# Kernel optimization log

Hardware: AMD Instinct MI355X
Metric: run time of the kernel (lower is better)

## Reference

```python
import jax, jax.numpy as jnp
import numpy as np

B, S, HID = 2, 4096, 2048
NH, NKV, HD = 16, 4, 128  # num_heads, num_kv_heads, head_dim
GROUPS = NH // NKV
ROPE_THETA = 10000.0


def _rope_cos_sin(position_ids):
    # position_ids: [B, S] int
    inv_freq = 1.0 / (ROPE_THETA ** (jnp.arange(0, HD, 2, dtype=jnp.float32) / HD))  # [HD/2]
    freqs = position_ids.astype(jnp.float32)[..., None] * inv_freq  # [B, S, HD/2]
    emb = jnp.concatenate([freqs, freqs], axis=-1)  # [B, S, HD]
    return jnp.cos(emb), jnp.sin(emb)


def _rotate_half(x):
    x1, x2 = jnp.split(x, 2, axis=-1)
    return jnp.concatenate([-x2, x1], axis=-1)


def _apply_rope(q, k, cos, sin):
    # q: [B, NH, S, HD], k: [B, NKV, S, HD]; cos/sin: [B, S, HD]
    cos = cos[:, None, :, :]
    sin = sin[:, None, :, :]
    q = q * cos + _rotate_half(q) * sin
    k = k * cos + _rotate_half(k) * sin
    return q, k


def kappa(x):
    return jax.nn.elu(x) + 1.0


def setup_inputs() -> dict:
    key = jax.random.key(0)
    ks = jax.random.split(key, 8)
    sc = 0.02
    hidden_states = jax.random.normal(ks[0], (B, S, HID), dtype=jnp.float32)
    position_ids = jnp.broadcast_to(jnp.arange(S, dtype=jnp.int64)[None, :], (B, S))
    Wq = jax.random.normal(ks[1], (HID, NH * HD), dtype=jnp.float32) * sc
    Wk = jax.random.normal(ks[2], (HID, NKV * HD), dtype=jnp.float32) * sc
    Wv = jax.random.normal(ks[3], (HID, NKV * HD), dtype=jnp.float32) * sc
    Wo = jax.random.normal(ks[4], (HID, HID), dtype=jnp.float32) * sc
    Wphi = jax.random.normal(ks[5], (HID, HID), dtype=jnp.float32) * sc
    bphi = jax.random.normal(ks[6], (HID,), dtype=jnp.float32) * sc
    return {"hidden_states": hidden_states, "position_ids": position_ids,
            "Wq": Wq, "Wk": Wk, "Wv": Wv, "Wo": Wo, "Wphi": Wphi, "bphi": bphi}


def reference(hidden_states, position_ids, Wq, Wk, Wv, Wo, Wphi, bphi):
    b, s, _ = hidden_states.shape
    # projections -> [B, heads, S, HD]
    q = (hidden_states @ Wq).reshape(b, s, NH, HD).transpose(0, 2, 1, 3)
    k = (hidden_states @ Wk).reshape(b, s, NKV, HD).transpose(0, 2, 1, 3)
    v = (hidden_states @ Wv).reshape(b, s, NKV, HD).transpose(0, 2, 1, 3)
    cos, sin = _rope_cos_sin(position_ids)
    q, k = _apply_rope(q, k, cos, sin)
    # GQA expand kv heads
    k = jnp.repeat(k, GROUPS, axis=1)  # [B, NH, S, HD]
    v = jnp.repeat(v, GROUPS, axis=1)
    Qk = kappa(q)
    Kk = kappa(k)
    Qg = Qk.mean(axis=2)  # [B, NH, HD]
    logits = jnp.einsum('bnd,bnsd->bns', Qg, Kk)
    alpha = jax.nn.softmax(logits, axis=-1) * float(s)  # [B, NH, S]
    outer_sum = jnp.einsum('bns,bnsd,bnsf->bndf', alpha, Kk, v)  # [B, NH, HD, HD]
    X_phi = (hidden_states @ Wphi + bphi).reshape(b, s, NH, HD).transpose(0, 2, 1, 3)
    result_attn = jnp.einsum('bnsd,bndf->bnsf', Qk, outer_sum)
    context = (X_phi * result_attn).transpose(0, 2, 1, 3).reshape(b, s, HID)
    return context @ Wo
```

## Files before the change

kernel.cpp:

```cpp
#include <hip/hip_runtime.h>
#include <hip/hip_bf16.h>
#include <math.h>

#define B_    2
#define S_    4096
#define HID_  2048
#define NH_   16
#define NKV_  4
#define HD_   128
#define GROUPS_ (NH_/NKV_)
#define ROPE_THETA_ 10000.0f
#define OSPLIT 8
#define QCH   32

typedef __attribute__((ext_vector_type(8))) short short8;
typedef __attribute__((ext_vector_type(4))) float f32x4;

__device__ inline unsigned short f2bf(float f) {
    __hip_bfloat16 h = __float2bfloat16(f);
    return *(unsigned short*)&h;
}

__device__ inline float bf2f(short u) {
    union { unsigned int i; float f; } v;
    v.i = ((unsigned int)(unsigned short)u) << 16;
    return v.f;
}

__device__ inline void gload16(const void* g, void* l) {
    __builtin_amdgcn_global_load_lds((const __attribute__((address_space(1))) void*)g,
                                     (__attribute__((address_space(3))) void*)l, 16, 0, 0);
}

#define BARM() asm volatile("s_barrier" ::: "memory")

__global__ void rope_table_kernel(float* __restrict__ cosT, float* __restrict__ sinT) {
    int s = blockIdx.x;
    int i = threadIdx.x;
    float expo = -2.0f * (float)i / (float)HD_;
    float invf = powf(ROPE_THETA_, expo);
    float f = (float)s * invf;
    cosT[s * 64 + i] = cosf(f);
    sinT[s * 64 + i] = sinf(f);
}

__global__ void cast_bf16_kernel(const float* __restrict__ in,
                                 __hip_bfloat16* __restrict__ out, int n8) {
    int i = blockIdx.x * 256 + threadIdx.x;
    if (i >= n8) return;
    const float4 v0 = *reinterpret_cast<const float4*>(&in[i * 8]);
    const float4 v1 = *reinterpret_cast<const float4*>(&in[i * 8 + 4]);
    union { short8 v; unsigned short u[8]; } o;
    o.u[0] = f2bf(v0.x); o.u[1] = f2bf(v0.y); o.u[2] = f2bf(v0.z); o.u[3] = f2bf(v0.w);
    o.u[4] = f2bf(v1.x); o.u[5] = f2bf(v1.y); o.u[6] = f2bf(v1.z); o.u[7] = f2bf(v1.w);
    *reinterpret_cast<short8*>(&out[i * 8]) = o.v;
}

__global__ __launch_bounds__(256) void transpose_cast_all_kernel(
        const float* __restrict__ W0, const float* __restrict__ W1,
        const float* __restrict__ W2, const float* __restrict__ W3,
        const float* __restrict__ W4, __hip_bfloat16* __restrict__ dstBase) {
    __shared__ float T[64][65];
    int id = blockIdx.x;
    const float* W; int N; size_t dof;
    if (id < 1024)      { W = W0; N = 2048; dof = 0; }
    else if (id < 1280) { W = W1; N = 512;  dof = (size_t)2048 * HID_;                  id -= 1024; }
    else if (id < 1536) { W = W2; N = 512;  dof = (size_t)(2048 + 512) * HID_;          id -= 1280; }
    else if (id < 2560) { W = W3; N = 2048; dof = (size_t)(2048 + 1024) * HID_;         id -= 1536; }
    else                { W = W4; N = 2048; dof = (size_t)(4096 + 1024) * HID_;         id -= 2560; }
    __hip_bfloat16* Wt = dstBase + dof;
    int nb = N >> 6;
    int n0 = (id % nb) * 64, k0 = (id / nb) * 64;
    int tid = threadIdx.x;
    int r = tid >> 4, c4 = (tid & 15) * 4;
#pragma unroll
    for (int p = 0; p < 4; ++p) {
        float4 v = *reinterpret_cast<const float4*>(&W[(size_t)(k0 + r + p * 16) * N + n0 + c4]);
        T[r + p * 16][c4 + 0] = v.x;
        T[r + p * 16][c4 + 1] = v.y;
        T[r + p * 16][c4 + 2] = v.z;
        T[r + p * 16][c4 + 3] = v.w;
    }
    __syncthreads();
#pragma unroll
    for (int p = 0; p < 4; ++p) {
        int n = r + p * 16;
        short4 o;
        o.x = (short)f2bf(T[c4 + 0][n]);
        o.y = (short)f2bf(T[c4 + 1][n]);
        o.z = (short)f2bf(T[c4 + 2][n]);
        o.w = (short)f2bf(T[c4 + 3][n]);
        *reinterpret_cast<short4*>(&Wt[(size_t)(n0 + n) * HID_ + k0 + c4]) = o;
    }
}

__device__ __forceinline__ void stage_region128(const __hip_bfloat16* __restrict__ src,
        int ldK, int row0, int kbase, __hip_bfloat16* dst, int tid) {
#pragma unroll
    for (int g = 0; g < 2; ++g) {
        int P = g * 256 + tid;
        int row = P >> 2, cp = P & 3;
        int cl = cp ^ ((row >> 1) & 3);
        gload16(src + (size_t)(row0 + row) * ldK + kbase + cl * 8, dst + P * 8);
    }
}

#define BM 128
#define BN 128
#define T128EL 8192
__global__ __launch_bounds__(256) void gemm_mfma_kernel(
        const __hip_bfloat16* __restrict__ A, const __hip_bfloat16* __restrict__ Bt,
        float* __restrict__ C, __hip_bfloat16* __restrict__ Cb,
        const float* __restrict__ bias, int M, int N, int K) {
    __shared__ __hip_bfloat16 lds[4 * T128EL];
    int tid  = threadIdx.x;
    int wid  = tid >> 6, lane = tid & 63;
    int wr   = wid >> 1, wc = wid & 1;
    int lr = lane & 15, lc = lane >> 4;
    int c16 = lc ^ ((lr >> 1) & 3);
    int bm = blockIdx.y * BM, bn = blockIdx.x * BN;

    f32x4 acc[4][4];
#pragma unroll
    for (int m = 0; m < 4; ++m)
#pragma unroll
        for (int n = 0; n < 4; ++n)
#pragma unroll
            for (int i = 0; i < 4; ++i) acc[m][n][i] = 0.0f;

    const int NKT = K >> 5;

    stage_region128(A,  K, bm, 0,  lds,                 tid);
    stage_region128(Bt, K, bn, 0,  lds + 4096,          tid);
    stage_region128(A,  K, bm, 32, lds + T128EL,        tid);
    stage_region128(Bt, K, bn, 32, lds + T128EL + 4096, tid);
    asm volatile("s_waitcnt vmcnt(4)" ::: "memory");
    BARM();

    for (int kt = 0; kt < NKT; ++kt) {
        __hip_bfloat16* buf = lds + (size_t)(kt & 3) * T128EL;
        __hip_bfloat16* stg = lds + (size_t)((kt + 2) & 3) * T128EL;
        const bool pf = (kt + 2 < NKT);
        if (pf) {
            stage_region128(A,  K, bm, (kt + 2) << 5, stg,        tid);
            stage_region128(Bt, K, bn, (kt + 2) << 5, stg + 4096, tid);
        }
        short8 af[4], bf[4];
#pragma unroll
        for (int m = 0; m < 4; ++m)
            af[m] = *reinterpret_cast<const short8*>(
                &buf[(size_t)(wr * 64 + m * 16 + lr) * 32 + c16 * 8]);
#pragma unroll
        for (int n = 0; n < 4; ++n)
            bf[n] = *reinterpret_cast<const short8*>(
                &buf[4096 + (size_t)(wc * 64 + n * 16 + lr) * 32 + c16 * 8]);
        __builtin_amdgcn_s_setprio(1);
#pragma unroll
        for (int m = 0; m < 4; ++m)
#pragma unroll
            for (int n = 0; n < 4; ++n)
                acc[m][n] = __builtin_amdgcn_mfma_f32_16x16x32_bf16(
                    af[m], bf[n], acc[m][n], 0, 0, 0);
        __builtin_amdgcn_s_setprio(0);
        if (pf) { asm volatile("s_waitcnt vmcnt(4)" ::: "memory"); }
        else    { asm volatile("s_waitcnt vmcnt(0)" ::: "memory"); }
        BARM();
    }

    int lq = lane >> 4;
#pragma unroll
    for (int m = 0; m < 4; ++m) {
#pragma unroll
        for (int n = 0; n < 4; ++n) {
            int row = bm + wr * 64 + m * 16 + lq * 4;
            int col = bn + wc * 64 + n * 16 + lr;
            float bv = (bias != nullptr) ? bias[col] : 0.0f;
            if (Cb != nullptr) {
#pragma unroll
                for (int r = 0; r < 4; ++r)
                    Cb[(size_t)(row + r) * N + col] = __float2bfloat16(acc[m][n][r] + bv);
            } else {
#pragma unroll
                for (int r = 0; r < 4; ++r)
                    C[(size_t)(row + r) * N + col] = acc[m][n][r] + bv;
            }
        }
    }
}

#define HBUF 32768

__device__ __forceinline__ void stageA64(const __hip_bfloat16* __restrict__ A,
        int ldK, int bm, int k0, __hip_bfloat16* dst, int g, int tid) {
    int P = g * 512 + tid;
    int row = P >> 3, sp = P & 7;
    gload16(A + (size_t)(bm + row) * ldK + k0 + ((sp ^ (row & 7)) << 3),
            dst + (size_t)P * 8);
}
__device__ __forceinline__ void stageB64(const __hip_bfloat16* __restrict__ Bt,
        int ldK, int bn, int k0, __hip_bfloat16* dst, int g, int tid) {
    int P = g * 512 + tid;
    int row = P >> 3, sp = P & 7;
    gload16(Bt + (size_t)(bn + row) * ldK + k0 + ((sp ^ (row & 7)) << 3),
            dst + 16384 + (size_t)P * 8);
}

__device__ __forceinline__ short8 ldsA64(const __hip_bfloat16* buf, int row, int slot_log) {
    int sp = slot_log ^ (row & 7);
    return *reinterpret_cast<const short8*>(&buf[(size_t)row * 64 + sp * 8]);
}
__device__ __forceinline__ short8 ldsB64(const __hip_bfloat16* buf, int row, int slot_log) {
    int sp = slot_log ^ (row & 7);
    return *reinterpret_cast<const short8*>(&buf[16384 + (size_t)row * 64 + sp * 8]);
}

__global__ __launch_bounds__(512, 2) void gemm_mfma256_kernel(
        const __hip_bfloat16* __restrict__ A, const __hip_bfloat16* __restrict__ Bt,
        float* __restrict__ C, __hip_bfloat16* __restrict__ Cb,
        const float* __restrict__ bias, int M, int N, int K) {
    __shared__ __hip_bfloat16 lds[2 * HBUF];
    int tid = threadIdx.x, lane = tid & 63, wid = tid >> 6;
    int wr = wid >> 2, wc = wid & 3;
    int lr = lane & 15, lc = lane >> 4;

    int nwg = gridDim.x;
    int orig = blockIdx.x;
    int q = nwg >> 3, r = nwg & 7;
    int xcd = orig & 7, lid = orig >> 3;
    int wg = (xcd < r ? xcd * (q + 1) : r * (q + 1) + (xcd - r) * q) + lid;
    int tiles_n = N >> 8;
    int bm = (wg / tiles_n) << 8, bn = (wg % tiles_n) << 8;

    f32x4 acc[8][4];
#pragma unroll
    for (int m = 0; m < 8; ++m)
#pragma unroll
        for (int n = 0; n < 4; ++n)
#pragma unroll
            for (int i = 0; i < 4; ++i) acc[m][n][i] = 0.0f;

    const int NKT = K >> 6;
    __hip_bfloat16* buf0 = lds;
    __hip_bfloat16* buf1 = lds + HBUF;

#pragma unroll
    for (int g = 0; g < 4; ++g) stageA64(A, K, bm, 0, buf0, g, tid);
#pragma unroll
    for (int g = 0; g < 4; ++g) stageB64(Bt, K, bn, 0, buf0, g, tid);
    stageA64(A, K, bm, 64, buf1, 0, tid);
    stageA64(A, K, bm, 64, buf1, 1, tid);
    asm volatile("s_waitcnt vmcnt(2)" ::: "memory");
    BARM();

    for (int kt = 0; kt < NKT; ++kt) {
        __hip_bfloat16* buf = (kt & 1) ? buf1 : buf0;
        __hip_bfloat16* nxt = (kt & 1) ? buf0 : buf1;
        const bool p1 = (kt + 1 < NKT), p2 = (kt + 2 < NKT);
        const int kn1 = (kt + 1) << 6;

        short8 al[4], ah[4], bl[2], bh[2];

#pragma unroll
        for (int kk = 0; kk < 2; ++kk) {
            int sl = kk * 4 + lc;
#pragma unroll
            for (int m = 0; m < 4; ++m)
                al[m] = ldsA64(buf, wr * 128 + m * 16 + lr, sl);
#pragma unroll
            for (int n = 0; n < 2; ++n)
                bl[n] = ldsB64(buf, wc * 64 + n * 16 + lr, sl);
            if (kk == 0 && p1) {
                stageA64(A, K, bm, kn1, nxt, 2, tid);
                stageA64(A, K, bm, kn1, nxt, 3, tid);
                stageB64(Bt, K, bn, kn1, nxt, 0, tid);
            }
            BARM();
            __builtin_amdgcn_s_setprio(1);
#pragma unroll
            for (int m = 0; m < 4; ++m)
#pragma unroll
                for (int n = 0; n < 2; ++n)
                    acc[m][n] = __builtin_amdgcn_mfma_f32_16x16x32_bf16(
                        al[m], bl[n], acc[m][n], 0, 0, 0);
            __builtin_amdgcn_s_setprio(0);
            BARM();
#pragma unroll
            for (int m = 0; m < 4; ++m)
                ah[m] = ldsA64(buf, wr * 128 + 64 + m * 16 + lr, sl);
            if (kk == 0 && p1) {
                stageB64(Bt, K, bn, kn1, nxt, 1, tid);
                stageB64(Bt, K, bn, kn1, nxt, 2, tid);
                stageB64(Bt, K, bn, kn1, nxt, 3, tid);
            }
            BARM();
            __builtin_amdgcn_s_setprio(1);
#pragma unroll
            for (int m = 0; m < 4; ++m)
#pragma unroll
                for (int n = 0; n < 2; ++n)
                    acc[m + 4][n] = __builtin_amdgcn_mfma_f32_16x16x32_bf16(
                        ah[m], bl[n], acc[m + 4][n], 0, 0, 0);
            __builtin_amdgcn_s_setprio(0);
            BARM();
#pragma unroll
            for (int n = 0; n < 2; ++n)
                bh[n] = ldsB64(buf, wc * 64 + (n + 2) * 16 + lr, sl);
            BARM();
            __builtin_amdgcn_s_setprio(1);
#pragma unroll
            for (int m = 0; m < 4; ++m)
#pragma unroll
                for (int n = 0; n < 2; ++n)
                    acc[m][n + 2] = __builtin_amdgcn_mfma_f32_16x16x32_bf16(
                        al[m], bh[n], acc[m][n + 2], 0, 0, 0);
            __builtin_amdgcn_s_setprio(0);
            BARM();
            if (kk == 1 && p2) {
                stageA64(A, K, bm, (kt + 2) << 6, buf, 0, tid);
                stageA64(A, K, bm, (kt + 2) << 6, buf, 1, tid);
            }
            __builtin_amdgcn_s_setprio(1);
#pragma unroll
            for (int m = 0; m < 4; ++m)
#pragma unroll
                for (int n = 0; n < 2; ++n)
                    acc[m + 4][n + 2] = __builtin_amdgcn_mfma_f32_16x16x32_bf16(
                        ah[m], bh[n], acc[m + 4][n + 2], 0, 0, 0);
            __builtin_amdgcn_s_setprio(0);
            if (kk == 1) {
                if (p2)      { asm volatile("s_waitcnt vmcnt(2)" ::: "memory"); }
                else if (p1) { asm volatile("s_waitcnt vmcnt(0)" ::: "memory"); }
                BARM();
            } else {
                BARM();
            }
        }
    }

    int lq = lane >> 4;
#pragma unroll
    for (int m = 0; m < 8; ++m) {
#pragma unroll
        for (int n = 0; n < 4; ++n) {
            int row = bm + wr * 128 + m * 16 + lq * 4;
            int col = bn + wc * 64 + n * 16 + lr;
            float bv = (bias != nullptr) ? bias[col] : 0.0f;
            if (Cb != nullptr) {
#pragma unroll
                for (int rr = 0; rr < 4; ++rr)
                    Cb[(size_t)(row + rr) * N + col] = __float2bfloat16(acc[m][n][rr] + bv);
            } else {
#pragma unroll
                for (int rr = 0; rr < 4; ++rr)
                    C[(size_t)(row + rr) * N + col] = acc[m][n][rr] + bv;
            }
        }
    }
}

__global__ void rope_kappa_b_kernel(__hip_bfloat16* __restrict__ Xb,
                                    const float* __restrict__ cosT,
                                    const float* __restrict__ sinT,
                                    int nheads, int rs, int total) {
    int idx = blockIdx.x * 256 + threadIdx.x;
    if (idx >= total) return;
    int dq = idx & 15;
    int t  = idx >> 4;
    int n  = t % nheads;
    int bs = t / nheads;
    int s  = bs % S_;
    size_t base = (size_t)bs * rs + n * HD_ + dq * 4;
    short4 v1 = *reinterpret_cast<short4*>(&Xb[base]);
    short4 v2 = *reinterpret_cast<short4*>(&Xb[base + 64]);
    float4 c4 = *reinterpret_cast<const float4*>(&cosT[s * 64 + dq * 4]);
    float4 s4 = *reinterpret_cast<const float4*>(&sinT[s * 64 + dq * 4]);
    float x1[4] = {bf2f(v1.x), bf2f(v1.y), bf2f(v1.z), bf2f(v1.w)};
    float x2[4] = {bf2f(v2.x), bf2f(v2.y), bf2f(v2.z), bf2f(v2.w)};
    float cc[4] = {c4.x, c4.y, c4.z, c4.w};
    float ss[4] = {s4.x, s4.y, s4.z, s4.w};
    short r1s[4], r2s[4];
#pragma unroll
    for (int j = 0; j < 4; ++j) {
        float r1 = x1[j] * cc[j] - x2[j] * ss[j];
        float r2 = x2[j] * cc[j] + x1[j] * ss[j];
        r1 = (r1 > 0.0f) ? (r1 + 1.0f) : expf(r1);
        r2 = (r2 > 0.0f) ? (r2 + 1.0f) : expf(r2);
        r1s[j] = (short)f2bf(r1);
        r2s[j] = (short)f2bf(r2);
    }
    short4 o1, o2;
    o1.x = r1s[0]; o1.y = r1s[1]; o1.z = r1s[2]; o1.w = r1s[3];
    o2.x = r2s[0]; o2.y = r2s[1]; o2.z = r2s[2]; o2.w = r2s[3];
    *reinterpret_cast<short4*>(&Xb[base])      = o1;
    *reinterpret_cast<short4*>(&Xb[base + 64]) = o2;
}

__global__ __launch_bounds__(256) void qg_partial_kernel(
        const __hip_bfloat16* __restrict__ Qb, float* __restrict__ QPART) {
    int blk = blockIdx.x;
    int c   = blk % QCH;
    int bn  = blk / QCH;
    int b = bn / NH_, n = bn % NH_;
    int t = threadIdx.x;
    int d8 = (t & 15) * 8;
    int sg = t >> 4;
    float acc[8] = {};
    int s0 = c * (S_ / QCH);
    for (int s = s0 + sg; s < s0 + S_ / QCH; s += 16) {
        short8 v = *reinterpret_cast<const short8*>(
            &Qb[((size_t)b * S_ + s) * (NH_ * HD_) + n * HD_ + d8]);
#pragma unroll
        for (int j = 0; j < 8; ++j) acc[j] += bf2f(v[j]);
    }
    __shared__ float red[16][128];
#pragma unroll
    for (int j = 0; j < 8; ++j) red[sg][d8 + j] = acc[j];
    __syncthreads();
    if (t < 128) {
        float s = 0.0f;
#pragma unroll
        for (int g = 0; g < 16; ++g) s += red[g][t];
        QPART[(size_t)(c * (B_ * NH_) + bn) * HD_ + t] = s;
    }
}

__global__ __launch_bounds__(256) void qg_reduce_kernel(
        const float* __restrict__ QPART, float* __restrict__ QG) {
    int idx = blockIdx.x * 256 + threadIdx.x;
    float acc = 0.0f;
#pragma unroll
    for (int c = 0; c < QCH; ++c)
        acc += QPART[(size_t)c * (B_ * NH_ * HD_) + idx];
    QG[idx] = acc * (1.0f / (float)S_);
}

__global__ __launch_bounds__(256) void logits_kernel(
        const __hip_bfloat16* __restrict__ KVb, const float* __restrict__ QG,
        float* __restrict__ LG) {
    int bk = blockIdx.x;
    int b = bk / NKV_, kn = bk % NKV_;
    int s0 = blockIdx.y * 256;
    int w = threadIdx.x >> 6, lane = threadIdx.x & 63;
    float2 qv[GROUPS_];
#pragma unroll
    for (int g = 0; g < GROUPS_; ++g)
        qv[g] = *reinterpret_cast<const float2*>(
            &QG[(size_t)(b * NH_ + kn * GROUPS_ + g) * HD_ + lane * 2]);
    for (int i = 0; i < 64; ++i) {
        int s = s0 + w * 64 + i;
        short2 kv = *reinterpret_cast<const short2*>(
            &KVb[((size_t)b * S_ + s) * 1024 + kn * HD_ + lane * 2]);
        float kx = bf2f(kv.x), ky = bf2f(kv.y);
        float p[GROUPS_];
#pragma unroll
        for (int g = 0; g < GROUPS_; ++g) p[g] = kx * qv[g].x + ky * qv[g].y;
#pragma unroll
        for (int off = 32; off > 0; off >>= 1)
#pragma unroll
            for (int g = 0; g < GROUPS_; ++g) p[g] += __shfl_xor(p[g], off);
        if (lane == 0) {
#pragma unroll
            for (int g = 0; g < GROUPS_; ++g)
                LG[(size_t)(b * NH_ + kn * GROUPS_ + g) * S_ + s] = p[g];
        }
    }
}

__global__ __launch_bounds__(1024) void softmax_alpha_kernel(float* __restrict__ LG) {
    int bn = blockIdx.x;
    float* row = &LG[(size_t)bn * S_];
    __shared__ float lg[S_];
    __shared__ float red[1024];
    int tid = threadIdx.x;
    float lmax = -1e30f;
    for (int s = tid; s < S_; s += 1024) {
        float v = row[s];
        lg[s] = v;
        lmax = fmaxf(lmax, v);
    }
    red[tid] = lmax;
    __syncthreads();
    for (int off = 512; off > 0; off >>= 1) {
        if (tid < off) red[tid] = fmaxf(red[tid], red[tid + off]);
        __syncthreads();
    }
    float mx = red[0];
    __syncthreads();
    float lsum = 0.0f;
    for (int s = tid; s < S_; s += 1024) {
        float e = expf(lg[s] - mx);
        lg[s] = e;
        lsum += e;
    }
    red[tid] = lsum;
    __syncthreads();
    for (int off = 512; off > 0; off >>= 1) {
        if (tid < off) red[tid] += red[tid + off];
        __syncthreads();
    }
    float inv = (float)S_ / red[0];
    for (int s = tid; s < S_; s += 1024)
        row[s] = lg[s] * inv;
}

__global__ __launch_bounds__(256) void kvt_kernel(
        const __hip_bfloat16* __restrict__ KVb, const float* __restrict__ ALPHA,
        __hip_bfloat16* __restrict__ AKT, __hip_bfloat16* __restrict__ VT) {
    int bk = blockIdx.x;
    int b = bk / NKV_, kn = bk % NKV_;
    int s0 = blockIdx.y * 64;
    int isV = blockIdx.z;
    __shared__ float T[64][HD_ + 4];
    __shared__ float alf[GROUPS_][64];
    int tid = threadIdx.x;

    int r = tid >> 2;
    int c0 = (tid & 3) * 32;
    const __hip_bfloat16* src =
        KVb + ((size_t)(b * S_) + s0 + r) * 1024 + isV * 512 + kn * HD_ + c0;
#pragma unroll
    for (int i = 0; i < 4; ++i) {
        short8 v = *reinterpret_cast<const short8*>(src + i * 8);
#pragma unroll
        for (int j = 0; j < 8; ++j) T[r][c0 + i * 8 + j] = bf2f(v[j]);
    }
    if (!isV) {
        int g = tid >> 6, ss = tid & 63;
        alf[g][ss] = ALPHA[(size_t)(b * NH_ + kn * GROUPS_ + g) * S_ + s0 + ss];
    }
    __syncthreads();

    int d  = tid >> 1;
    int sh = (tid & 1) * 32;
    if (isV) {
        __hip_bfloat16* dst = VT + ((size_t)bk * HD_ + d) * S_ + s0 + sh;
#pragma unroll
        for (int i = 0; i < 8; ++i) {
            short4 o;
            o.x = (short)f2bf(T[sh + i * 4 + 0][d]);
            o.y = (short)f2bf(T[sh + i * 4 + 1][d]);
            o.z = (short)f2bf(T[sh + i * 4 + 2][d]);
            o.w = (short)f2bf(T[sh + i * 4 + 3][d]);
            *reinterpret_cast<short4*>(dst + i * 4) = o;
        }
    } else {
#pragma unroll
        for (int g = 0; g < GROUPS_; ++g) {
            int n = kn * GROUPS_ + g;
            __hip_bfloat16* dst = AKT + ((size_t)(b * NH_ + n) * HD_ + d) * S_ + s0 + sh;
#pragma unroll
            for (int i = 0; i < 8; ++i) {
                short4 o;
                o.x = (short)f2bf(T[sh + i * 4 + 0][d] * alf[g][sh + i * 4 + 0]);
                o.y = (short)f2bf(T[sh + i * 4 + 1][d] * alf[g][sh + i * 4 + 1]);
                o.z = (short)f2bf(T[sh + i * 4 + 2][d] * alf[g][sh + i * 4 + 2]);
                o.w = (short)f2bf(T[sh + i * 4 + 3][d] * alf[g][sh + i * 4 + 3]);
                *reinterpret_cast<short4*>(dst + i * 4) = o;
            }
        }
    }
}

__global__ __launch_bounds__(256) void outer_mfma_kernel(
        const __hip_bfloat16* __restrict__ AKT, const __hip_bfloat16* __restrict__ VT,
        float* __restrict__ OPT) {
    int bn = blockIdx.x;
    int sp = blockIdx.y;
    int b = bn / NH_, n = bn % NH_;
    int kn = n / GROUPS_;
    const __hip_bfloat16* Abase = AKT + (size_t)bn * HD_ * S_ + sp * (S_ / OSPLIT);
    const __hip_bfloat16* Bbase = VT + (size_t)(b * NKV_ + kn) * HD_ * S_ + sp * (S_ / OSPLIT);
    __shared__ __hip_bfloat16 As[128 * 32];
    __shared__ __hip_bfloat16 Bs[128 * 32];
    int tid = threadIdx.x, lane = tid & 63, wid = tid >> 6;
    int wr = wid >> 1, wc = wid & 1;
    int lr = lane & 15, kq = (lane >> 4) * 8;

    f32x4 acc[4][4];
#pragma unroll
    for (int m = 0; m < 4; ++m)
#pragma unroll
        for (int nn = 0; nn < 4; ++nn)
#pragma unroll
            for (int i = 0; i < 4; ++i) acc[m][nn][i] = 0.0f;

    for (int ks = 0; ks < (S_ / OSPLIT) / 32; ++ks) {
        int k0 = ks * 32;
#pragma unroll
        for (int g = 0; g < 2; ++g) {
            int P = g * 256 + tid;
            int row = P >> 2, gr = P & 3;
            gload16(Abase + (size_t)row * S_ + k0 + gr * 8, As + P * 8);
            gload16(Bbase + (size_t)row * S_ + k0 + gr * 8, Bs + P * 8);
        }
        __syncthreads();
        short8 af[4], bf[4];
#pragma unroll
        for (int m = 0; m < 4; ++m)
            af[m] = *reinterpret_cast<short8*>(&As[(wr * 64 + m * 16 + lr) * 32 + kq]);
#pragma unroll
        for (int nn = 0; nn < 4; ++nn)
            bf[nn] = *reinterpret_cast<short8*>(&Bs[(wc * 64 + nn * 16 + lr) * 32 + kq]);
#pragma unroll
        for (int m = 0; m < 4; ++m)
#pragma unroll
            for (int nn = 0; nn < 4; ++nn)
                acc[m][nn] = __builtin_amdgcn_mfma_f32_16x16x32_bf16(
                    af[m], bf[nn], acc[m][nn], 0, 0, 0);
        __syncthreads();
    }

    float* base = OPT + ((size_t)bn * OSPLIT + sp) * (HD_ * HD_);
    int lq = lane >> 4;
#pragma unroll
    for (int m = 0; m < 4; ++m) {
#pragma unroll
        for (int nn = 0; nn < 4; ++nn) {
            int drow = wr * 64 + m * 16 + lq * 4;
            int fcol = wc * 64 + nn * 16 + lr;
            float4 o;
            o.x = acc[m][nn][0]; o.y = acc[m][nn][1];
            o.z = acc[m][nn][2]; o.w = acc[m][nn][3];
            *reinterpret_cast<float4*>(&base[(size_t)fcol * HD_ + drow]) = o;
        }
    }
}

__global__ __launch_bounds__(256) void outer_reduce_tc_kernel(
        const float* __restrict__ OPT, __hip_bfloat16* __restrict__ OUTt) {
    int idx = blockIdx.x * 256 + threadIdx.x;
    int bn = idx >> 11;
    int rem = idx & 2047;
    int f = rem >> 4, g = rem & 15;
    const float* src = OPT + (size_t)bn * OSPLIT * 16384 + f * 128 + g * 8;
    float s[8] = {};
#pragma unroll
    for (int sp = 0; sp < OSPLIT; ++sp) {
        float4 v0 = *reinterpret_cast<const float4*>(src + (size_t)sp * 16384);
        float4 v1 = *reinterpret_cast<const float4*>(src + (size_t)sp * 16384 + 4);
        s[0] += v0.x; s[1] += v0.y; s[2] += v0.z; s[3] += v0.w;
        s[4] += v1.x; s[5] += v1.y; s[6] += v1.z; s[7] += v1.w;
    }
    int gp = g ^ (f & 7);
    union { short8 v; unsigned short u[8]; } o;
#pragma unroll
    for (int j = 0; j < 8; ++j) o.u[j] = f2bf(s[j]);
    *reinterpret_cast<short8*>(&OUTt[(size_t)bn * 16384 + f * 128 + gp * 8]) = o.v;
}

__global__ __launch_bounds__(256) void attn_context_mfma_kernel(
        const __hip_bfloat16* __restrict__ Qb, const __hip_bfloat16* __restrict__ OUTt,
        const __hip_bfloat16* __restrict__ XPHIb, __hip_bfloat16* __restrict__ CTX) {
    int bn = blockIdx.x;
    int b = bn / NH_, n = bn % NH_;
    int s0 = blockIdx.y * 256;
    __shared__ __hip_bfloat16 Ms[128 * 128];
    int tid = threadIdx.x, lane = tid & 63, wid = tid >> 6;
    int lr = lane & 15, lc = lane >> 4;

#pragma unroll
    for (int g = 0; g < 8; ++g) {
        int P = g * 256 + tid;
        gload16(OUTt + (size_t)bn * 16384 + (size_t)P * 8, Ms + (size_t)P * 8);
    }

    f32x4 acc[4][8];
#pragma unroll
    for (int m = 0; m < 4; ++m)
#pragma unroll
        for (int nn = 0; nn < 8; ++nn)
#pragma unroll
            for (int i = 0; i < 4; ++i) acc[m][nn][i] = 0.0f;

    __syncthreads();

    const __hip_bfloat16* qbase =
        Qb + ((size_t)(b * S_) + s0 + wid * 64) * (NH_ * HD_) + n * HD_;
#pragma unroll
    for (int ks = 0; ks < 4; ++ks) {
        int k8 = ks * 32 + lc * 8;
        short8 a[4];
#pragma unroll
        for (int m = 0; m < 4; ++m)
            a[m] = *reinterpret_cast<const short8*>(
                qbase + (size_t)(m * 16 + lr) * (NH_ * HD_) + k8);
        int gfull = ks * 4 + lc;
        short8 bb[8];
#pragma unroll
        for (int nn = 0; nn < 8; ++nn) {
            int f = nn * 16 + lr;
            int gp = gfull ^ (f & 7);
            bb[nn] = *reinterpret_cast<const short8*>(&Ms[f * 128 + gp * 8]);
        }
#pragma unroll
        for (int m = 0; m < 4; ++m)
#pragma unroll
            for (int nn = 0; nn < 8; ++nn)
                acc[m][nn] = __builtin_amdgcn_mfma_f32_16x16x32_bf16(
                    a[m], bb[nn], acc[m][nn], 0, 0, 0);
    }

#pragma unroll
    for (int m = 0; m < 4; ++m) {
#pragma unroll
        for (int nn = 0; nn < 8; ++nn) {
            int row = s0 + wid * 64 + m * 16 + lc * 4;
            int f = nn * 16 + lr;
            size_t gi = ((size_t)(b * S_) + row) * (NH_ * HD_) + n * HD_ + f;
#pragma unroll
            for (int r = 0; r < 4; ++r) {
                float xp = __bfloat162float(XPHIb[gi + (size_t)r * (NH_ * HD_)]);
                CTX[gi + (size_t)r * (NH_ * HD_)] = __float2bfloat16(acc[m][nn][r] * xp);
            }
        }
    }
}

extern "C" void kernel_launch(void* const* d_in, const int* in_sizes, int n_in,
                              void* d_out, int out_size, void* d_ws, size_t ws_size,
                              hipStream_t stream) {
    (void)in_sizes; (void)n_in; (void)out_size; (void)ws_size;
    const float* X    = (const float*)d_in[0];
    const float* Wq   = (const float*)d_in[2];
    const float* Wk   = (const float*)d_in[3];
    const float* Wv   = (const float*)d_in[4];
    const float* Wo   = (const float*)d_in[5];
    const float* Wphi = (const float*)d_in[6];
    const float* bphi = (const float*)d_in[7];
    float* out = (float*)d_out;

    float* ws = (float*)d_ws;
    const size_t nQ = (size_t)B_ * S_ * NH_ * HD_;
    const size_t nK = (size_t)B_ * S_ * NKV_ * HD_;
    float* Q     = ws;
    float* KV    = Q + nQ;
    float* XPHI  = KV + 2 * nK;
    float* QG    = XPHI + nQ;
    float* ALPHA = QG + (size_t)B_ * NH_ * HD_;
    float* QPART = ALPHA + (size_t)B_ * NH_ * S_;
    float* COST  = QPART + (size_t)QCH * B_ * NH_ * HD_;
    float* SINT  = COST + (size_t)S_ * 64;
    __hip_bfloat16* Xb    = (__hip_bfloat16*)(SINT + (size_t)S_ * 64);
    __hip_bfloat16* Wqt   = Xb + nQ;
    __hip_bfloat16* Wkt   = Wqt + (size_t)HID_ * (NH_ * HD_);
    __hip_bfloat16* Wvt   = Wkt + (size_t)HID_ * (NKV_ * HD_);
    __hip_bfloat16* Wphit = Wvt + (size_t)HID_ * (NKV_ * HD_);
    __hip_bfloat16* Wot   = Wphit + (size_t)HID_ * (NH_ * HD_);
    __hip_bfloat16* OUTt  = Wot + (size_t)HID_ * HID_;
    __hip_bfloat16* VT    = OUTt + (size_t)B_ * NH_ * HD_ * HD_;
    float* OPT = (float*)(VT + nK);
    __hip_bfloat16* Qb    = (__hip_bfloat16*)Q;
    __hip_bfloat16* KVb   = (__hip_bfloat16*)KV;
    __hip_bfloat16* CTXb  = (__hip_bfloat16*)KV;
    __hip_bfloat16* AKT   = Xb;
    __hip_bfloat16* XPHIb = (__hip_bfloat16*)XPHI;

    const int M = B_ * S_;

    rope_table_kernel<<<S_, 64, 0, stream>>>(COST, SINT);
    cast_bf16_kernel<<<(int)(nQ / 8 / 256), 256, 0, stream>>>(X, Xb, (int)(nQ / 8));
    transpose_cast_all_kernel<<<3584, 256, 0, stream>>>(Wq, Wk, Wv, Wphi, Wo, Wqt);

    gemm_mfma256_kernel<<<(M / 256) * ((NH_ * HD_) / 256), 512, 0, stream>>>(
        Xb, Wqt, nullptr, Qb, nullptr, M, NH_ * HD_, HID_);
    gemm_mfma_kernel<<<dim3(1024 / BN, M / BM), 256, 0, stream>>>(
        Xb, Wkt, nullptr, KVb, nullptr, M, 1024, HID_);
    gemm_mfma256_kernel<<<(M / 256) * ((NH_ * HD_) / 256), 512, 0, stream>>>(
        Xb, Wphit, nullptr, XPHIb, bphi, M, NH_ * HD_, HID_);

    {
        int totalQ = B_ * S_ * NH_ * 16;
        rope_kappa_b_kernel<<<totalQ / 256, 256, 0, stream>>>(
            Qb, COST, SINT, NH_, NH_ * HD_, totalQ);
        int totalK = B_ * S_ * NKV_ * 16;
        rope_kappa_b_kernel<<<totalK / 256, 256, 0, stream>>>(
            KVb, COST, SINT, NKV_, 1024, totalK);
    }

    qg_partial_kernel<<<B_ * NH_ * QCH, 256, 0, stream>>>(Qb, QPART);
    qg_reduce_kernel<<<(B_ * NH_ * HD_) / 256, 256, 0, stream>>>(QPART, QG);
    logits_kernel<<<dim3(B_ * NKV_, S_ / 256), 256, 0, stream>>>(KVb, QG, ALPHA);
    softmax_alpha_kernel<<<B_ * NH_, 1024, 0, stream>>>(ALPHA);

    kvt_kernel<<<dim3(B_ * NKV_, S_ / 64, 2), 256, 0, stream>>>(KVb, ALPHA, AKT, VT);
    outer_mfma_kernel<<<dim3(B_ * NH_, OSPLIT), 256, 0, stream>>>(AKT, VT, OPT);
    outer_reduce_tc_kernel<<<(B_ * NH_ * HD_ * 16) / 256, 256, 0, stream>>>(OPT, OUTt);

    attn_context_mfma_kernel<<<dim3(B_ * NH_, S_ / 256), 256, 0, stream>>>(
        Qb, OUTt, XPHIb, CTXb);

    gemm_mfma256_kernel<<<(M / 256) * (HID_ / 256), 512, 0, stream>>>(
        CTXb, Wot, out, nullptr, nullptr, M, HID_, HID_);
}
```

Before: 419.2 us.

## Merge Q and Xphi projections into one GEMM and fuse RoPE-kappa with Q mean

Q and Wphi weights are now transposed into one contiguous [4096 x HID] bf16 matrix, so a single 256x256-tile GEMM with N=4096 computes both projections. The epilogue sends each column tile to the Q or Xphi buffer and adds the bias only on the Xphi half. Separately, the Q RoPE+kappa pass is fused with the per-chunk Q column partial sums, which removes one full read of Q. The intent is to cut a kernel launch and a tail wave and to avoid re-reading the large Q tensor. The cost is a per-tile branch in the epilogue and a less coalesced access pattern in the fused RoPE kernel.

```diff
diff --git a/kernel.cpp b/kernel.cpp
--- a/kernel.cpp
+++ b/kernel.cpp
@@ -57,17 +57,17 @@
 }
 
 __global__ __launch_bounds__(256) void transpose_cast_all_kernel(
-        const float* __restrict__ W0, const float* __restrict__ W1,
-        const float* __restrict__ W2, const float* __restrict__ W3,
-        const float* __restrict__ W4, __hip_bfloat16* __restrict__ dstBase) {
+        const float* __restrict__ Wq, const float* __restrict__ Wphi,
+        const float* __restrict__ Wk, const float* __restrict__ Wv,
+        const float* __restrict__ Wo, __hip_bfloat16* __restrict__ dstBase) {
     __shared__ float T[64][65];
     int id = blockIdx.x;
     const float* W; int N; size_t dof;
-    if (id < 1024)      { W = W0; N = 2048; dof = 0; }
-    else if (id < 1280) { W = W1; N = 512;  dof = (size_t)2048 * HID_;                  id -= 1024; }
-    else if (id < 1536) { W = W2; N = 512;  dof = (size_t)(2048 + 512) * HID_;          id -= 1280; }
-    else if (id < 2560) { W = W3; N = 2048; dof = (size_t)(2048 + 1024) * HID_;         id -= 1536; }
-    else                { W = W4; N = 2048; dof = (size_t)(4096 + 1024) * HID_;         id -= 2560; }
+    if (id < 1024)      { W = Wq;   N = 2048; dof = 0; }
+    else if (id < 2048) { W = Wphi; N = 2048; dof = (size_t)2048 * HID_;        id -= 1024; }
+    else if (id < 2304) { W = Wk;   N = 512;  dof = (size_t)4096 * HID_;        id -= 2048; }
+    else if (id < 2560) { W = Wv;   N = 512;  dof = (size_t)(4096 + 512) * HID_; id -= 2304; }
+    else                { W = Wo;   N = 2048; dof = (size_t)5120 * HID_;        id -= 2560; }
     __hip_bfloat16* Wt = dstBase + dof;
     int nb = N >> 6;
     int n0 = (id % nb) * 64, k0 = (id / nb) * 64;
@@ -110,8 +110,7 @@
 #define T128EL 8192
 __global__ __launch_bounds__(256) void gemm_mfma_kernel(
         const __hip_bfloat16* __restrict__ A, const __hip_bfloat16* __restrict__ Bt,
-        float* __restrict__ C, __hip_bfloat16* __restrict__ Cb,
-        const float* __restrict__ bias, int M, int N, int K) {
+        __hip_bfloat16* __restrict__ Cb, int M, int N, int K) {
     __shared__ __hip_bfloat16 lds[4 * T128EL];
     int tid  = threadIdx.x;
     int wid  = tid >> 6, lane = tid & 63;
@@ -174,16 +173,9 @@
         for (int n = 0; n < 4; ++n) {
             int row = bm + wr * 64 + m * 16 + lq * 4;
             int col = bn + wc * 64 + n * 16 + lr;
-            float bv = (bias != nullptr) ? bias[col] : 0.0f;
-            if (Cb != nullptr) {
-#pragma unroll
-                for (int r = 0; r < 4; ++r)
-                    Cb[(size_t)(row + r) * N + col] = __float2bfloat16(acc[m][n][r] + bv);
-            } else {
-#pragma unroll
-                for (int r = 0; r < 4; ++r)
-                    C[(size_t)(row + r) * N + col] = acc[m][n][r] + bv;
-            }
+#pragma unroll
+            for (int r = 0; r < 4; ++r)
+                Cb[(size_t)(row + r) * N + col] = __float2bfloat16(acc[m][n][r]);
         }
     }
 }
@@ -216,8 +208,9 @@
 
 __global__ __launch_bounds__(512, 2) void gemm_mfma256_kernel(
         const __hip_bfloat16* __restrict__ A, const __hip_bfloat16* __restrict__ Bt,
-        float* __restrict__ C, __hip_bfloat16* __restrict__ Cb,
-        const float* __restrict__ bias, int M, int N, int K) {
+        float* __restrict__ C, __hip_bfloat16* __restrict__ CbQ,
+        __hip_bfloat16* __restrict__ CbP, const float* __restrict__ bias,
+        int M, int N, int K) {
     __shared__ __hip_bfloat16 lds[2 * HBUF];
     int tid = threadIdx.x, lane = tid & 63, wid = tid >> 6;
     int wr = wid >> 2, wc = wid & 3;
@@ -338,24 +331,94 @@
     }
 
     int lq = lane >> 4;
-#pragma unroll
-    for (int m = 0; m < 8; ++m) {
-#pragma unroll
-        for (int n = 0; n < 4; ++n) {
-            int row = bm + wr * 128 + m * 16 + lq * 4;
-            int col = bn + wc * 64 + n * 16 + lr;
-            float bv = (bias != nullptr) ? bias[col] : 0.0f;
-            if (Cb != nullptr) {
+    if (CbQ != nullptr) {
+        bool isQ = (bn < 2048);
+        __hip_bfloat16* dst = isQ ? CbQ : CbP;
+        int cb = isQ ? bn : bn - 2048;
+#pragma unroll
+        for (int m = 0; m < 8; ++m) {
+#pragma unroll
+            for (int n = 0; n < 4; ++n) {
+                int row = bm + wr * 128 + m * 16 + lq * 4;
+                int col = cb + wc * 64 + n * 16 + lr;
+                float bv = isQ ? 0.0f : bias[col];
 #pragma unroll
                 for (int rr = 0; rr < 4; ++rr)
-                    Cb[(size_t)(row + rr) * N + col] = __float2bfloat16(acc[m][n][rr] + bv);
-            } else {
+                    dst[(size_t)(row + rr) * 2048 + col] = __float2bfloat16(acc[m][n][rr] + bv);
+            }
+        }
+    } else {
+#pragma unroll
+        for (int m = 0; m < 8; ++m) {
+#pragma unroll
+            for (int n = 0; n < 4; ++n) {
+                int row = bm + wr * 128 + m * 16 + lq * 4;
+                int col = bn + wc * 64 + n * 16 + lr;
 #pragma unroll
                 for (int rr = 0; rr < 4; ++rr)
-                    C[(size_t)(row + rr) * N + col] = acc[m][n][rr] + bv;
+                    C[(size_t)(row + rr) * N + col] = acc[m][n][rr];
             }
         }
     }
+}
+
+__global__ __launch_bounds__(256) void rope_qg_kernel(
+        __hip_bfloat16* __restrict__ Qb, const float* __restrict__ cosT,
+        const float* __restrict__ sinT, float* __restrict__ QPART) {
+    int blk = blockIdx.x;
+    int c = blk % QCH, bn = blk / QCH;
+    int b = bn / NH_, n = bn % NH_;
+    int tid = threadIdx.x;
+    int pg = tid & 7;
+    int sg = tid >> 3;
+    int s0 = c * (S_ / QCH);
+    float acc1[8] = {}, acc2[8] = {};
+    for (int sr = sg; sr < S_ / QCH; sr += 32) {
+        int s = s0 + sr;
+        size_t base = ((size_t)b * S_ + s) * (NH_ * HD_) + n * HD_ + pg * 8;
+        short8 v1 = *reinterpret_cast<short8*>(&Qb[base]);
+        short8 v2 = *reinterpret_cast<short8*>(&Qb[base + 64]);
+        union { short8 v; unsigned short u[8]; } o1, o2;
+#pragma unroll
+        for (int j = 0; j < 8; ++j) {
+            float cc = cosT[s * 64 + pg * 8 + j];
+            float ss = sinT[s * 64 + pg * 8 + j];
+            float x1 = bf2f(v1[j]), x2 = bf2f(v2[j]);
+            float r1 = x1 * cc - x2 * ss;
+            float r2 = x2 * cc + x1 * ss;
+            r1 = (r1 > 0.0f) ? (r1 + 1.0f) : expf(r1);
+            r2 = (r2 > 0.0f) ? (r2 + 1.0f) : expf(r2);
+            o1.u[j] = f2bf(r1);
+            o2.u[j] = f2bf(r2);
+            acc1[j] += bf2f((short)o1.u[j]);
+            acc2[j] += bf2f((short)o2.u[j]);
+        }
+        *reinterpret_cast<short8*>(&Qb[base])      = o1.v;
+        *reinterpret_cast<short8*>(&Qb[base + 64]) = o2.v;
+    }
+    __shared__ float red[32][128];
+#pragma unroll
+    for (int j = 0; j < 8; ++j) {
+        red[sg][pg * 8 + j]      = acc1[j];
+        red[sg][64 + pg * 8 + j] = acc2[j];
+    }
+    __syncthreads();
+    if (tid < 128) {
+        float s = 0.0f;
+#pragma unroll
+        for (int g = 0; g < 32; ++g) s += red[g][tid];
+        QPART[(size_t)(c * (B_ * NH_) + bn) * HD_ + tid] = s;
+    }
+}
+
+__global__ __launch_bounds__(256) void qg_reduce_kernel(
+        const float* __restrict__ QPART, float* __restrict__ QG) {
+    int idx = blockIdx.x * 256 + threadIdx.x;
+    float acc = 0.0f;
+#pragma unroll
+    for (int c = 0; c < QCH; ++c)
+        acc += QPART[(size_t)c * (B_ * NH_ * HD_) + idx];
+    QG[idx] = acc * (1.0f / (float)S_);
 }
 
 __global__ void rope_kappa_b_kernel(__hip_bfloat16* __restrict__ Xb,
@@ -395,45 +458,6 @@
     *reinterpret_cast<short4*>(&Xb[base + 64]) = o2;
 }
 
-__global__ __launch_bounds__(256) void qg_partial_kernel(
-        const __hip_bfloat16* __restrict__ Qb, float* __restrict__ QPART) {
-    int blk = blockIdx.x;
-    int c   = blk % QCH;
-    int bn  = blk / QCH;
-    int b = bn / NH_, n = bn % NH_;
-    int t = threadIdx.x;
-    int d8 = (t & 15) * 8;
-    int sg = t >> 4;
-    float acc[8] = {};
-    int s0 = c * (S_ / QCH);
-    for (int s = s0 + sg; s < s0 + S_ / QCH; s += 16) {
-        short8 v = *reinterpret_cast<const short8*>(
-            &Qb[((size_t)b * S_ + s) * (NH_ * HD_) + n * HD_ + d8]);
-#pragma unroll
-        for (int j = 0; j < 8; ++j) acc[j] += bf2f(v[j]);
-    }
-    __shared__ float red[16][128];
-#pragma unroll
-    for (int j = 0; j < 8; ++j) red[sg][d8 + j] = acc[j];
-    __syncthreads();
-    if (t < 128) {
-        float s = 0.0f;
-#pragma unroll
-        for (int g = 0; g < 16; ++g) s += red[g][t];
-        QPART[(size_t)(c * (B_ * NH_) + bn) * HD_ + t] = s;
-    }
-}
-
-__global__ __launch_bounds__(256) void qg_reduce_kernel(
-        const float* __restrict__ QPART, float* __restrict__ QG) {
-    int idx = blockIdx.x * 256 + threadIdx.x;
-    float acc = 0.0f;
-#pragma unroll
-    for (int c = 0; c < QCH; ++c)
-        acc += QPART[(size_t)c * (B_ * NH_ * HD_) + idx];
-    QG[idx] = acc * (1.0f / (float)S_);
-}
-
 __global__ __launch_bounds__(256) void logits_kernel(
         const __hip_bfloat16* __restrict__ KVb, const float* __restrict__ QG,
         float* __restrict__ LG) {
@@ -740,14 +764,12 @@
     float* QPART = ALPHA + (size_t)B_ * NH_ * S_;
     float* COST  = QPART + (size_t)QCH * B_ * NH_ * HD_;
     float* SINT  = COST + (size_t)S_ * 64;
-    __hip_bfloat16* Xb    = (__hip_bfloat16*)(SINT + (size_t)S_ * 64);
-    __hip_bfloat16* Wqt   = Xb + nQ;
-    __hip_bfloat16* Wkt   = Wqt + (size_t)HID_ * (NH_ * HD_);
-    __hip_bfloat16* Wvt   = Wkt + (size_t)HID_ * (NKV_ * HD_);
-    __hip_bfloat16* Wphit = Wvt + (size_t)HID_ * (NKV_ * HD_);
-    __hip_bfloat16* Wot   = Wphit + (size_t)HID_ * (NH_ * HD_);
-    __hip_bfloat16* OUTt  = Wot + (size_t)HID_ * HID_;
-    __hip_bfloat16* VT    = OUTt + (size_t)B_ * NH_ * HD_ * HD_;
+    __hip_bfloat16* Xb     = (__hip_bfloat16*)(SINT + (size_t)S_ * 64);
+    __hip_bfloat16* WqPhit = Xb + nQ;
+    __hip_bfloat16* Wkt    = WqPhit + (size_t)4096 * HID_;
+    __hip_bfloat16* Wot    = WqPhit + (size_t)5120 * HID_;
+    __hip_bfloat16* OUTt   = Wot + (size_t)HID_ * HID_;
+    __hip_bfloat16* VT     = OUTt + (size_t)B_ * NH_ * HD_ * HD_;
     float* OPT = (float*)(VT + nK);
     __hip_bfloat16* Qb    = (__hip_bfloat16*)Q;
     __hip_bfloat16* KVb   = (__hip_bfloat16*)KV;
@@ -759,25 +781,20 @@
 
     rope_table_kernel<<<S_, 64, 0, stream>>>(COST, SINT);
     cast_bf16_kernel<<<(int)(nQ / 8 / 256), 256, 0, stream>>>(X, Xb, (int)(nQ / 8));
-    transpose_cast_all_kernel<<<3584, 256, 0, stream>>>(Wq, Wk, Wv, Wphi, Wo, Wqt);
-
-    gemm_mfma256_kernel<<<(M / 256) * ((NH_ * HD_) / 256), 512, 0, stream>>>(
-        Xb, Wqt, nullptr, Qb, nullptr, M, NH_ * HD_, HID_);
+    transpose_cast_all_kernel<<<3584, 256, 0, stream>>>(Wq, Wphi, Wk, Wv, Wo, WqPhit);
+
+    gemm_mfma256_kernel<<<(M / 256) * (4096 / 256), 512, 0, stream>>>(
+        Xb, WqPhit, nullptr, Qb, XPHIb, bphi, M, 4096, HID_);
     gemm_mfma_kernel<<<dim3(1024 / BN, M / BM), 256, 0, stream>>>(
-        Xb, Wkt, nullptr, KVb, nullptr, M, 1024, HID_);
-    gemm_mfma256_kernel<<<(M / 256) * ((NH_ * HD_) / 256), 512, 0, stream>>>(
-        Xb, Wphit, nullptr, XPHIb, bphi, M, NH_ * HD_, HID_);
-
+        Xb, Wkt, KVb, M, 1024, HID_);
+
+    rope_qg_kernel<<<B_ * NH_ * QCH, 256, 0, stream>>>(Qb, COST, SINT, QPART);
     {
-        int totalQ = B_ * S_ * NH_ * 16;
-        rope_kappa_b_kernel<<<totalQ / 256, 256, 0, stream>>>(
-            Qb, COST, SINT, NH_, NH_ * HD_, totalQ);
         int totalK = B_ * S_ * NKV_ * 16;
         rope_kappa_b_kernel<<<totalK / 256, 256, 0, stream>>>(
             KVb, COST, SINT, NKV_, 1024, totalK);
     }
 
-    qg_partial_kernel<<<B_ * NH_ * QCH, 256, 0, stream>>>(Qb, QPART);
     qg_reduce_kernel<<<(B_ * NH_ * HD_) / 256, 256, 0, stream>>>(QPART, QG);
     logits_kernel<<<dim3(B_ * NKV_, S_ / 256), 256, 0, stream>>>(KVb, QG, ALPHA);
     softmax_alpha_kernel<<<B_ * NH_, 1024, 0, stream>>>(ALPHA);
@@ -790,5 +807,5 @@
         Qb, OUTt, XPHIb, CTXb);
 
     gemm_mfma256_kernel<<<(M / 256) * (HID_ / 256), 512, 0, stream>>>(
-        CTXb, Wot, out, nullptr, nullptr, M, HID_, HID_);
-}
+        CTXb, Wot, out, nullptr, nullptr, nullptr, M, HID_, HID_);
+}
```

Measured after the change: 409.7 us. -2.3%, faster.
